# Optimization experiments

Measured on AMD Instinct MI355X. Metric: run time of the kernel, lower is better.

The kernel has to match this reference:

```python
import jax, jax.numpy as jnp
import numpy as np

LAMBDA_S = 1.0   # options['lambda_s']
NITER = 100      # options['iter_ihs']

_HS_FILTER = jnp.array([[1/12, 1/6, 1/12],
                        [1/6,  0.0, 1/6 ],
                        [1/12, 1/6, 1/12]], dtype=jnp.float32)


def _smooth(f):
    # f: [n, h, w] -> 3x3 Horn-Schunck weighted average, zero padding (== torch conv2d padding=1)
    k = _HS_FILTER.reshape(1, 1, 3, 3)  # [out_c, in_c, kh, kw]
    return jax.lax.conv_general_dilated(f[:, None], k, window_strides=(1, 1), padding='SAME')[:, 0]


def setup_inputs() -> dict:
    key = jax.random.key(0)
    k1, k2 = jax.random.split(key)
    n, h, w = 8, 256, 256
    x = jax.random.normal(k1, (n, 3, h, w), dtype=jnp.float32)            # [I_t, I_x, I_y]
    old_estimate = jax.random.normal(k2, (n, 2, h, w), dtype=jnp.float32)  # warm-start (u, v)
    return {"x": x, "old_estimate": old_estimate}


def reference(x, old_estimate):
    # x: [n,3,h,w]; old_estimate: [n,2,h,w]
    I_t, I_x, I_y = x[:, 0], x[:, 1], x[:, 2]
    denom = LAMBDA_S ** 2 + I_x ** 2 + I_y ** 2  # iteration-invariant
    u0, v0 = old_estimate[:, 0], old_estimate[:, 1]  # warm_ihs=True

    def step(carry, _):
        u, v = carry
        u_bar = _smooth(u)
        v_bar = _smooth(v)
        der = (I_x * u_bar + I_y * v_bar + I_t) / denom
        return (u_bar - I_x * der, v_bar - I_y * der), None

    (u, v), _ = jax.lax.scan(step, (u0, v0), None, length=NITER)
    return jnp.stack((u, v), axis=1)  # [n,2,h,w]
```

## Files before the change

### kernel.cpp

```cpp
#include <hip/hip_runtime.h>

typedef unsigned long long ull;
typedef float f32x2 __attribute__((ext_vector_type(2)));
#define FMA2(a,b,c) __builtin_elementwise_fma((a),(b),(c))

#define HH 256
#define WW 256
#define PLANE (HH*WW)
#define TILE_R 32
#define TILE_C 64
#define TT 8
#define ER (TILE_R + 2*TT)
#define EC (TILE_C + 2*TT)
#define NCP (EC/2)
#define NRG 16
#define RPT (ER/NRG)
#define NTHR 1024
#define STRIDE 164
#define LSZ (4 + ER*STRIDE + 4)
#define HROW (NCP*4)
#define HBUFSZ (2*NRG*2*HROW)

#define RING_OFS (2u*1024u*1024u)
#define FLAG_OFS (4u*1024u*1024u)
#define RIMG (HH*(WW/2)*4)
#define NBLK 256

__device__ __forceinline__ float dpp_prev(float v) {
    return __int_as_float(__builtin_amdgcn_update_dpp(0, __float_as_int(v), 0x138, 0xF, 0xF, true));
}
__device__ __forceinline__ float dpp_next(float v) {
    return __int_as_float(__builtin_amdgcn_update_dpp(0, __float_as_int(v), 0x130, 0xF, 0xF, true));
}

__device__ __forceinline__ void hsum2(const float4 M, f32x2& S0, f32x2& S1) {
    f32x2 lo = { M.x, M.y }, hi = { M.z, M.w };
    f32x2 DL = { dpp_prev(M.z), dpp_prev(M.w) };
    f32x2 DR = { dpp_next(M.x), dpp_next(M.y) };
    const f32x2 two = 2.0f;
    S0 = FMA2(two, lo, DL) + hi;
    S1 = FMA2(two, hi, lo) + DR;
}

__device__ __forceinline__ void do_step(
    int q, float* __restrict__ hbuf,
    bool act, int rg, int cp, int r0,
    float4* __restrict__ Mreg,
    const f32x2 (* __restrict__ CA)[2], const f32x2 (* __restrict__ CB)[2],
    const f32x2 (* __restrict__ CC)[2])
{
    const int par = (q - 1) & 1;
    const bool on = act && (r0 + RPT - 1 >= q - 1) && (r0 <= 48 - q);
    f32x2 S0[RPT+2], S1[RPT+2];

    if (on) {
        #pragma unroll
        for (int j = 0; j < RPT; ++j) hsum2(Mreg[j], S0[j+1], S1[j+1]);
        float* hb = hbuf + (par*NRG + rg)*2*HROW + 4*cp;
        *(float4*)(hb)        = make_float4(S0[1].x,   S0[1].y,   S1[1].x,   S1[1].y);
        *(float4*)(hb + HROW) = make_float4(S0[RPT].x, S0[RPT].y, S1[RPT].x, S1[RPT].y);
    }
    __syncthreads();
    if (on) {
        if (rg > 0) {
            float4 t = *(const float4*)(hbuf + ((par*NRG + rg-1)*2 + 1)*HROW + 4*cp);
            S0[0] = (f32x2){t.x, t.y}; S1[0] = (f32x2){t.z, t.w};
        } else { S0[0] = S0[1]; S1[0] = S1[1]; }
        if (rg < NRG-1) {
            float4 t = *(const float4*)(hbuf + ((par*NRG + rg+1)*2 + 0)*HROW + 4*cp);
            S0[RPT+1] = (f32x2){t.x, t.y}; S1[RPT+1] = (f32x2){t.z, t.w};
        } else { S0[RPT+1] = S0[RPT]; S1[RPT+1] = S1[RPT]; }

        const f32x2 two = 2.0f, m4 = -4.0f;
        #pragma unroll
        for (int j = 0; j < RPT; ++j) {
            float4 Mc = Mreg[j];
            f32x2 Mlo = { Mc.x, Mc.y }, Mhi = { Mc.z, Mc.w };
            f32x2 T0 = FMA2(m4, Mlo, FMA2(two, S0[j+1], S0[j]) + S0[j+2]);
            f32x2 T1 = FMA2(m4, Mhi, FMA2(two, S1[j+1], S1[j]) + S1[j+2]);
            f32x2 rr0 = FMA2(CA[j][0], T0, -FMA2(CB[j][0], T0.yx, CC[j][0]));
            f32x2 rr1 = FMA2(CA[j][1], T1, -FMA2(CB[j][1], T1.yx, CC[j][1]));
            Mreg[j] = make_float4(rr0.x, rr0.y, rr1.x, rr1.y);
        }
    }
}

__global__ __launch_bounds__(NTHR, 4)
void hs_mega(const float* __restrict__ x,
             const float* __restrict__ est,
             float* __restrict__ out,
             float* __restrict__ ws)
{
    __shared__ __align__(16) float sraw[LSZ];
    __shared__ __align__(16) float hbuf[HBUFSZ];

    const int img = blockIdx.x, cs = blockIdx.y, rb = blockIdx.z;
    const int tid = threadIdx.x;
    const int er0 = rb*TILE_R - TT;
    const int ec0 = cs*TILE_C - TT;
    const int blin = (img*4 + cs)*8 + rb;
    unsigned* flags = (unsigned*)(ws + FLAG_OFS);

    int nb = -1;
    if (tid < 8) {
        int t = (tid < 4) ? tid : tid + 1;
        int dr = t/3 - 1, dc = t%3 - 1;
        int nrb = rb + dr, ncs = cs + dc;
        if (nrb >= 0 && nrb < 8 && ncs >= 0 && ncs < 4)
            nb = (img*4 + ncs)*8 + nrb;
    }

    const int cp = tid & 63;
    const int rg = tid >> 6;
    const bool act = (cp < NCP);
    const int r0 = rg * RPT;
    const int fb = 4 + 4*cp;

    f32x2 CA[RPT][2], CB[RPT][2], CC[RPT][2];
    if (act) {
        const float* __restrict__ xit = x + img*3*PLANE;
        const float* __restrict__ xix = xit + PLANE;
        const float* __restrict__ xiy = xix + PLANE;
        #pragma unroll
        for (int i = 0; i < RPT; ++i) {
            int gr = er0 + r0 + i;
            #pragma unroll
            for (int j = 0; j < 2; ++j) {
                int gc = ec0 + 2*cp + j;
                float A=0.f, B=0.f, C=0.f, D=0.f, E=0.f;
                if (gr >= 0 && gr < HH && gc >= 0 && gc < WW) {
                    int q = gr*WW + gc;
                    float it = xit[q], ix = xix[q], iy = xiy[q];
                    float rd = 1.0f / (1.0f + ix*ix + iy*iy);
                    const float s12 = 1.0f/12.0f;
                    A = (1.0f - ix*ix*rd) * s12;
                    B = (ix*iy*rd) * s12;
                    C = ix*it*rd;
                    D = (1.0f - iy*iy*rd) * s12;
                    E = iy*it*rd;
                }
                CA[i][j] = (f32x2){ A, D };
                CB[i][j] = (f32x2){ B, B };
                CC[i][j] = (f32x2){ C, E };
            }
        }
    }

    {
        const float* __restrict__ eu = est + img*2*PLANE;
        const float* __restrict__ ev = eu + PLANE;
        for (int k = tid; k < ER*NCP; k += NTHR) {
            int r = k / NCP, c = k - r*NCP;
            int gr = er0 + r, gc = ec0 + 2*c;
            float2 uu = make_float2(0.f,0.f), vv = make_float2(0.f,0.f);
            if (gr >= 0 && gr < HH && gc >= 0 && gc < WW) {
                uu = *(const float2*)(eu + gr*WW + gc);
                vv = *(const float2*)(ev + gr*WW + gc);
            }
            *(float4*)(sraw + 4 + STRIDE*r + 4*c) = make_float4(uu.x, vv.x, uu.y, vv.y);
        }
    }
    __syncthreads();

    float4 Mreg[RPT];
    if (act) {
        #pragma unroll
        for (int j = 0; j < RPT; ++j)
            Mreg[j] = *(const float4*)(sraw + STRIDE*(r0 + j) + fb);
    }

    for (int p = 0; p < 13; ++p) {
        if (p < 12) {
            #pragma unroll
            for (int q = 1; q <= 8; ++q)
                do_step(q, hbuf, act, rg, cp, r0, Mreg, CA, CB, CC);
        } else {
            #pragma unroll
            for (int q = 1; q <= 4; ++q)
                do_step(q, hbuf, act, rg, cp, r0, Mreg, CA, CB, CC);
        }

        if (p < 12) {
            float* ring = ws + (unsigned)(p & 1) * RING_OFS + img*RIMG;

            if (act) {
                #pragma unroll
                for (int j = 0; j < RPT; ++j) {
                    int r = r0 + j;
                    int rr = r - TT, cc = cp - 4;
                    bool inner = (rr >= 0 && rr < TILE_R && cc >= 0 && cc < TILE_C/2);
                    if (inner && (rr < 8 || rr >= TILE_R-8 || cc < 4 || cc >= TILE_C/2-4)) {
                        union { float4 f; ull u[2]; } U; U.f = Mreg[j];
                        float* gp = ring + ((rb*TILE_R + rr)*(WW/2) + cs*(TILE_C/2) + cc)*4;
                        __hip_atomic_store((ull*)gp,     U.u[0], __ATOMIC_RELAXED, __HIP_MEMORY_SCOPE_AGENT);
                        __hip_atomic_store((ull*)gp + 1, U.u[1], __ATOMIC_RELAXED, __HIP_MEMORY_SCOPE_AGENT);
                    }
                }
            }
            asm volatile("s_waitcnt vmcnt(0)" ::: "memory");
            __syncthreads();
            if (tid == 0)
                __hip_atomic_store(&flags[p*NBLK + blin], 0x5eed0100u + (unsigned)p,
                                   __ATOMIC_RELAXED, __HIP_MEMORY_SCOPE_AGENT);
            asm volatile("" ::: "memory");
            if (tid < 8 && nb >= 0) {
                const unsigned tgt = 0x5eed0100u + (unsigned)p;
                while (__hip_atomic_load(&flags[p*NBLK + nb],
                                         __ATOMIC_RELAXED, __HIP_MEMORY_SCOPE_AGENT) != tgt)
                    __builtin_amdgcn_s_sleep(1);
            }
            __syncthreads();

            if (act) {
                #pragma unroll
                for (int j = 0; j < RPT; ++j) {
                    int r = r0 + j;
                    if (r < TT || r >= ER-TT || cp < 4 || cp >= NCP-4) {
                        int gr = er0 + r, gc2 = cs*(TILE_C/2) - 4 + cp;
                        if (gr >= 0 && gr < HH && gc2 >= 0 && gc2 < WW/2) {
                            const float* gp = ring + (gr*(WW/2) + gc2)*4;
                            union { float4 f; ull u[2]; } U;
                            U.u[0] = __hip_atomic_load((const ull*)gp,     __ATOMIC_RELAXED, __HIP_MEMORY_SCOPE_AGENT);
                            U.u[1] = __hip_atomic_load((const ull*)gp + 1, __ATOMIC_RELAXED, __HIP_MEMORY_SCOPE_AGENT);
                            Mreg[j] = U.f;
                        } else {
                            Mreg[j] = make_float4(0.f, 0.f, 0.f, 0.f);
                        }
                    }
                }
            }
        }
    }

    {
        float* ou = out + img*2*PLANE;
        float* ov = ou + PLANE;
        if (act) {
            #pragma unroll
            for (int j = 0; j < RPT; ++j) {
                int r = r0 + j;
                int rr = r - TT, cc = cp - 4;
                if (rr >= 0 && rr < TILE_R && cc >= 0 && cc < TILE_C/2) {
                    int qq = (rb*TILE_R + rr)*WW + cs*TILE_C + 2*cc;
                    *(float2*)(ou + qq) = make_float2(Mreg[j].x, Mreg[j].z);
                    *(float2*)(ov + qq) = make_float2(Mreg[j].y, Mreg[j].w);
                }
            }
        }
    }
}

extern "C" void kernel_launch(void* const* d_in, const int* in_sizes, int n_in,
                              void* d_out, int out_size, void* d_ws, size_t ws_size,
                              hipStream_t stream) {
    const float* x   = (const float*)d_in[0];
    const float* est = (const float*)d_in[1];
    float* out = (float*)d_out;
    float* ws  = (float*)d_ws;

    dim3 grid(8, WW/TILE_C, HH/TILE_R);
    dim3 blk(NTHR);
    hs_mega<<<grid, blk, 0, stream>>>(x, est, out, ws);
}
```

Baseline: 179.0 us.

## Double temporal tile depth and stage halo exchange through shared memory

Raises the temporal blocking depth from 8 to 16 steps per exchange, so inter-block halo exchanges and flag spin-waits drop from 12 to 6 rounds. This widens the tile's halo region, which adds redundant computation and registers per thread. Global ring writes, halo reads and final output writes are staged through one shared buffer (sraw, hbuf and xbuf now alias) so the global accesses become contiguous per thread. The aliasing needs the extra barriers that were added.

New measurement: 168.9 us. 5.6% less time.

```diff
diff --git a/kernel.cpp b/kernel.cpp
--- a/kernel.cpp
+++ b/kernel.cpp
@@ -9,14 +9,14 @@
 #define PLANE (HH*WW)
 #define TILE_R 32
 #define TILE_C 64
-#define TT 8
+#define TT 16
 #define ER (TILE_R + 2*TT)
 #define EC (TILE_C + 2*TT)
 #define NCP (EC/2)
 #define NRG 16
 #define RPT (ER/NRG)
 #define NTHR 1024
-#define STRIDE 164
+#define STRIDE 196
 #define LSZ (4 + ER*STRIDE + 4)
 #define HROW (NCP*4)
 #define HBUFSZ (2*NRG*2*HROW)
@@ -25,6 +25,7 @@
 #define FLAG_OFS (4u*1024u*1024u)
 #define RIMG (HH*(WW/2)*4)
 #define NBLK 256
+#define NHALO (ER*NCP - TILE_R*(TILE_C/2))
 
 __device__ __forceinline__ float dpp_prev(float v) {
     return __int_as_float(__builtin_amdgcn_update_dpp(0, __float_as_int(v), 0x138, 0xF, 0xF, true));
@@ -50,7 +51,7 @@
     const f32x2 (* __restrict__ CC)[2])
 {
     const int par = (q - 1) & 1;
-    const bool on = act && (r0 + RPT - 1 >= q - 1) && (r0 <= 48 - q);
+    const bool on = act && (r0 + RPT - 1 >= q - 1) && (r0 <= ER - q);
     f32x2 S0[RPT+2], S1[RPT+2];
 
     if (on) {
@@ -85,14 +86,22 @@
     }
 }
 
+__device__ __forceinline__ int halo_idx(int r, int cp) {
+    if (r < TT)       return r*NCP + cp;
+    if (r >= ER-TT)   return TT*NCP + (r-(ER-TT))*NCP + cp;
+    return 2*TT*NCP + (r-TT)*(2*(TT/2)) + ((cp < TT/2) ? cp : cp - (NCP-TT/2) + TT/2);
+}
+
 __global__ __launch_bounds__(NTHR, 4)
 void hs_mega(const float* __restrict__ x,
              const float* __restrict__ est,
              float* __restrict__ out,
              float* __restrict__ ws)
 {
-    __shared__ __align__(16) float sraw[LSZ];
-    __shared__ __align__(16) float hbuf[HBUFSZ];
+    __shared__ __align__(16) float smem[LSZ];
+    float* const sraw = smem;
+    float* const hbuf = smem;
+    float* const xbuf = smem;
 
     const int img = blockIdx.x, cs = blockIdx.y, rb = blockIdx.z;
     const int tid = threadIdx.x;
@@ -168,11 +177,12 @@
         for (int j = 0; j < RPT; ++j)
             Mreg[j] = *(const float4*)(sraw + STRIDE*(r0 + j) + fb);
     }
-
-    for (int p = 0; p < 13; ++p) {
-        if (p < 12) {
+    __syncthreads();
+
+    for (int p = 0; p < 7; ++p) {
+        if (p < 6) {
             #pragma unroll
-            for (int q = 1; q <= 8; ++q)
+            for (int q = 1; q <= 16; ++q)
                 do_step(q, hbuf, act, rg, cp, r0, Mreg, CA, CB, CC);
         } else {
             #pragma unroll
@@ -180,22 +190,25 @@
                 do_step(q, hbuf, act, rg, cp, r0, Mreg, CA, CB, CC);
         }
 
-        if (p < 12) {
+        if (p < 6) {
             float* ring = ws + (unsigned)(p & 1) * RING_OFS + img*RIMG;
 
+            __syncthreads();
             if (act) {
                 #pragma unroll
                 for (int j = 0; j < RPT; ++j) {
-                    int r = r0 + j;
-                    int rr = r - TT, cc = cp - 4;
-                    bool inner = (rr >= 0 && rr < TILE_R && cc >= 0 && cc < TILE_C/2);
-                    if (inner && (rr < 8 || rr >= TILE_R-8 || cc < 4 || cc >= TILE_C/2-4)) {
-                        union { float4 f; ull u[2]; } U; U.f = Mreg[j];
-                        float* gp = ring + ((rb*TILE_R + rr)*(WW/2) + cs*(TILE_C/2) + cc)*4;
-                        __hip_atomic_store((ull*)gp,     U.u[0], __ATOMIC_RELAXED, __HIP_MEMORY_SCOPE_AGENT);
-                        __hip_atomic_store((ull*)gp + 1, U.u[1], __ATOMIC_RELAXED, __HIP_MEMORY_SCOPE_AGENT);
-                    }
-                }
+                    int rr = r0 + j - TT, cc = cp - TT/2;
+                    if (rr >= 0 && rr < TILE_R && cc >= 0 && cc < TILE_C/2)
+                        *(float4*)(xbuf + 4*(rr*(TILE_C/2) + cc)) = Mreg[j];
+                }
+            }
+            __syncthreads();
+            for (int k = tid; k < TILE_R*(TILE_C/2); k += NTHR) {
+                int r = k >> 5, c2 = k & 31;
+                const float* sp = xbuf + 4*k;
+                float* gp = ring + ((rb*TILE_R + r)*(WW/2) + cs*(TILE_C/2) + c2)*4;
+                __hip_atomic_store((ull*)gp,     *(const ull*)sp,       __ATOMIC_RELAXED, __HIP_MEMORY_SCOPE_AGENT);
+                __hip_atomic_store((ull*)gp + 1, *(const ull*)(sp + 2), __ATOMIC_RELAXED, __HIP_MEMORY_SCOPE_AGENT);
             }
             asm volatile("s_waitcnt vmcnt(0)" ::: "memory");
             __syncthreads();
@@ -211,41 +224,54 @@
             }
             __syncthreads();
 
+            for (int k = tid; k < NHALO; k += NTHR) {
+                int r, c2;
+                if (k < TT*NCP)            { r = k / NCP;                 c2 = k - (k/NCP)*NCP; }
+                else if (k < 2*TT*NCP)     { int m = k - TT*NCP; r = (ER-TT) + m/NCP; c2 = m - (m/NCP)*NCP; }
+                else { int m = k - 2*TT*NCP; r = TT + m/TT; int t = m % TT; c2 = (t < TT/2) ? t : (NCP-TT/2) + (t-TT/2); }
+                int gr = er0 + r, gc2 = cs*(TILE_C/2) - TT/2 + c2;
+                ull v0 = 0, v1 = 0;
+                if (gr >= 0 && gr < HH && gc2 >= 0 && gc2 < WW/2) {
+                    const float* gp = ring + (gr*(WW/2) + gc2)*4;
+                    v0 = __hip_atomic_load((const ull*)gp,     __ATOMIC_RELAXED, __HIP_MEMORY_SCOPE_AGENT);
+                    v1 = __hip_atomic_load((const ull*)gp + 1, __ATOMIC_RELAXED, __HIP_MEMORY_SCOPE_AGENT);
+                }
+                float* sp = xbuf + 4*k;
+                *(ull*)sp = v0;
+                *(ull*)(sp + 2) = v1;
+            }
+            __syncthreads();
             if (act) {
                 #pragma unroll
                 for (int j = 0; j < RPT; ++j) {
                     int r = r0 + j;
-                    if (r < TT || r >= ER-TT || cp < 4 || cp >= NCP-4) {
-                        int gr = er0 + r, gc2 = cs*(TILE_C/2) - 4 + cp;
-                        if (gr >= 0 && gr < HH && gc2 >= 0 && gc2 < WW/2) {
-                            const float* gp = ring + (gr*(WW/2) + gc2)*4;
-                            union { float4 f; ull u[2]; } U;
-                            U.u[0] = __hip_atomic_load((const ull*)gp,     __ATOMIC_RELAXED, __HIP_MEMORY_SCOPE_AGENT);
-                            U.u[1] = __hip_atomic_load((const ull*)gp + 1, __ATOMIC_RELAXED, __HIP_MEMORY_SCOPE_AGENT);
-                            Mreg[j] = U.f;
-                        } else {
-                            Mreg[j] = make_float4(0.f, 0.f, 0.f, 0.f);
-                        }
-                    }
-                }
-            }
-        }
-    }
-
+                    if (r < TT || r >= ER-TT || cp < TT/2 || cp >= NCP-TT/2)
+                        Mreg[j] = *(const float4*)(xbuf + 4*halo_idx(r, cp));
+                }
+            }
+            __syncthreads();
+        }
+    }
+
+    __syncthreads();
+    if (act) {
+        #pragma unroll
+        for (int j = 0; j < RPT; ++j) {
+            int rr = r0 + j - TT, cc = cp - TT/2;
+            if (rr >= 0 && rr < TILE_R && cc >= 0 && cc < TILE_C/2)
+                *(float4*)(xbuf + 4*(rr*(TILE_C/2) + cc)) = Mreg[j];
+        }
+    }
+    __syncthreads();
     {
         float* ou = out + img*2*PLANE;
         float* ov = ou + PLANE;
-        if (act) {
-            #pragma unroll
-            for (int j = 0; j < RPT; ++j) {
-                int r = r0 + j;
-                int rr = r - TT, cc = cp - 4;
-                if (rr >= 0 && rr < TILE_R && cc >= 0 && cc < TILE_C/2) {
-                    int qq = (rb*TILE_R + rr)*WW + cs*TILE_C + 2*cc;
-                    *(float2*)(ou + qq) = make_float2(Mreg[j].x, Mreg[j].z);
-                    *(float2*)(ov + qq) = make_float2(Mreg[j].y, Mreg[j].w);
-                }
-            }
+        for (int k = tid; k < TILE_R*(TILE_C/2); k += NTHR) {
+            int r = k >> 5, c2 = k & 31;
+            float4 V = *(const float4*)(xbuf + 4*k);
+            int q = (rb*TILE_R + r)*WW + cs*TILE_C + 2*c2;
+            *(float2*)(ou + q) = make_float2(V.x, V.z);
+            *(float2*)(ov + q) = make_float2(V.y, V.w);
         }
     }
 }
```
